# Kernel optimization log

Hardware: AMD Instinct MI355X
Metric: run time of the kernel (lower is better)

The kernel has to match this reference:

```python
import jax, jax.numpy as jnp
import numpy as np

B, F, N, L, K = 16, 256, 16384, 4096, 9  # batch, channels, input pixels, pooled pixels, kernel


def setup_inputs() -> dict:
    key = jax.random.key(0)
    k1, k2 = jax.random.split(key, 2)
    input_images = jax.random.normal(k1, (B, F, N), dtype=jnp.float32)
    # raw indices in [-1, N-1]; -1 marks a missing neighbor (zero padding)
    raw = jax.random.randint(k2, (L, K), 0, N + 1) - 1
    mask = (raw != -1).astype(jnp.float32)          # prepare_mask: mask out -1 entries
    indices = jnp.maximum(raw, 0)                   # prepare_mask: clamp -1 -> 0
    return {"input_images": input_images, "indices": indices, "mask": mask}


def reference(input_images, indices, mask):
    # gather neighbor features: (B, F, L, K)
    col = input_images[..., indices] * mask
    # max over kernel (neighbor) axis -> pooled image (B, F, L)
    return jnp.max(col, axis=-1)
```

## Files before the change

### kernel.cpp

```cpp
#include <hip/hip_runtime.h>

#define B_ 16
#define F_ 256
#define N_ 16384
#define L_ 4096
#define K_ 9

#define NTHR 256

typedef const __attribute__((address_space(1))) void* gas_ptr;
typedef __attribute__((address_space(3))) void* las_ptr;

__global__ __launch_bounds__(256) void prep_comb_kernel(
    const int* __restrict__ idx, const float* __restrict__ mask,
    unsigned short* __restrict__ comb) {
  int t = blockIdx.x * blockDim.x + threadIdx.x;
  if (t >= L_ * K_) return;
  int l = t / K_;
  int k = t - l * K_;
  comb[k * L_ + l] =
      (mask[t] != 0.0f) ? (unsigned short)idx[t] : (unsigned short)N_;
}

__global__ __launch_bounds__(NTHR) void pool_kernel(
    const float* __restrict__ img, const unsigned short* __restrict__ comb,
    float* __restrict__ out) {
  __shared__ __align__(16) float row[N_ + 4];
  const int bf = blockIdx.x;
  const int tid = threadIdx.x;
  const int lane = tid & 63;
  const int wv = tid >> 6;

  const float* src = img + (size_t)bf * N_;
#pragma unroll
  for (int i = 0; i < 16; ++i) {
    const int c = i * 4 + wv;
    const float* g = src + c * 256 + lane * 4;
    __builtin_amdgcn_global_load_lds((gas_ptr)g, (las_ptr)(row + c * 256),
                                     16, 0, 0);
  }
  if (tid == 0) row[N_] = 0.0f;
  __syncthreads();

  float* outp = out + (size_t)bf * L_;
#pragma unroll
  for (int it = 0; it < L_ / NTHR; ++it) {
    int l = it * NTHR + tid;
    float m = -INFINITY;
#pragma unroll
    for (int k = 0; k < K_; ++k) {
      int id = comb[k * L_ + l];
      m = fmaxf(m, row[id]);
    }
    outp[l] = m;
  }
}

__global__ __launch_bounds__(256) void pool_kernel_direct(
    const float* __restrict__ img, const int* __restrict__ idx,
    const float* __restrict__ mask, float* __restrict__ out) {
  __shared__ __align__(16) float row[N_ + 4];
  const int bf = blockIdx.x;
  const int tid = threadIdx.x;

  const float4* src4 = (const float4*)(img + (size_t)bf * N_);
  float4* row4 = (float4*)row;
#pragma unroll
  for (int i = 0; i < 16; ++i) {
    int j = i * 256 + tid;
    row4[j] = src4[j];
  }
  __syncthreads();

  float* outp = out + (size_t)bf * L_;
  for (int it = 0; it < L_ / 256; ++it) {
    int l = it * 256 + tid;
    float m = -INFINITY;
#pragma unroll
    for (int k = 0; k < K_; ++k) {
      int t = l * K_ + k;
      float v = (mask[t] != 0.0f) ? row[idx[t]] : 0.0f;
      m = fmaxf(m, v);
    }
    outp[l] = m;
  }
}

extern "C" void kernel_launch(void* const* d_in, const int* in_sizes, int n_in,
                              void* d_out, int out_size, void* d_ws, size_t ws_size,
                              hipStream_t stream) {
  const float* img = (const float*)d_in[0];
  const int* idx = (const int*)d_in[1];
  const float* mask = (const float*)d_in[2];
  float* out = (float*)d_out;

  const size_t comb_bytes = (size_t)L_ * K_ * sizeof(unsigned short);
  if (ws_size >= comb_bytes) {
    unsigned short* comb = (unsigned short*)d_ws;
    int total = L_ * K_;
    prep_comb_kernel<<<(total + 255) / 256, 256, 0, stream>>>(idx, mask, comb);
    pool_kernel<<<B_ * F_, NTHR, 0, stream>>>(img, comb, out);
  } else {
    pool_kernel_direct<<<B_ * F_, 256, 0, stream>>>(img, idx, mask, out);
  }
}
```

Before: 79.64 us.

## Make pooling kernel persistent with double-buffered LDS row prefetch

Replaces the one-block-per-(batch,channel) launch with 256 persistent 1024-thread blocks. Each block handles 16 rows, and the async global-to-LDS load of the next row overlaps with the gather/max over the current row in a second LDS buffer. The 9-way max is also rebalanced into a shallower tree after all gathers are issued. The aim is to hide row-load latency and cut per-block launch and ramp-up costs. In exchange, 128KB of LDS per block allows only one block per CU, and each row step needs a block-wide barrier.

```diff
diff --git a/kernel.cpp b/kernel.cpp
--- a/kernel.cpp
+++ b/kernel.cpp
@@ -6,7 +6,9 @@
 #define L_ 4096
 #define K_ 9
 
-#define NTHR 256
+#define NTHR 1024
+#define NBLK 256
+#define ROWS_PER_BLK (B_ * F_ / NBLK)
 
 typedef const __attribute__((address_space(1))) void* gas_ptr;
 typedef __attribute__((address_space(3))) void* las_ptr;
@@ -22,38 +24,57 @@
       (mask[t] != 0.0f) ? (unsigned short)idx[t] : (unsigned short)N_;
 }
 
-__global__ __launch_bounds__(NTHR) void pool_kernel(
+__global__ __launch_bounds__(NTHR) void pool_pipe_kernel(
     const float* __restrict__ img, const unsigned short* __restrict__ comb,
     float* __restrict__ out) {
-  __shared__ __align__(16) float row[N_ + 4];
-  const int bf = blockIdx.x;
+  __shared__ __align__(16) float buf[2][N_ + 16];
   const int tid = threadIdx.x;
+  const int bid = blockIdx.x;
   const int lane = tid & 63;
   const int wv = tid >> 6;
 
-  const float* src = img + (size_t)bf * N_;
-#pragma unroll
-  for (int i = 0; i < 16; ++i) {
-    const int c = i * 4 + wv;
-    const float* g = src + c * 256 + lane * 4;
-    __builtin_amdgcn_global_load_lds((gas_ptr)g, (las_ptr)(row + c * 256),
-                                     16, 0, 0);
+#define STAGE_ROW(row_, dstbuf_)                                         \
+  {                                                                      \
+    const float* src_ = img + (size_t)(row_)*N_;                         \
+    _Pragma("unroll") for (int i_ = 0; i_ < 4; ++i_) {                   \
+      const int c_ = i_ * 16 + wv;                                       \
+      __builtin_amdgcn_global_load_lds((gas_ptr)(src_ + c_ * 256 + lane * 4), \
+                                       (las_ptr)((dstbuf_) + c_ * 256),  \
+                                       16, 0, 0);                        \
+    }                                                                    \
   }
-  if (tid == 0) row[N_] = 0.0f;
+
+  STAGE_ROW(bid, &buf[0][0]);
+  if (tid < 2) buf[tid][N_] = 0.0f;
   __syncthreads();
 
-  float* outp = out + (size_t)bf * L_;
+#pragma unroll 1
+  for (int p = 0; p < ROWS_PER_BLK; ++p) {
+    if (p + 1 < ROWS_PER_BLK) {
+      const int nrow = (p + 1) * NBLK + bid;
+      STAGE_ROW(nrow, &buf[(p + 1) & 1][0]);
+    }
+
+    const float* row = &buf[p & 1][0];
+    float* outp = out + (size_t)((size_t)p * NBLK + bid) * L_;
 #pragma unroll
-  for (int it = 0; it < L_ / NTHR; ++it) {
-    int l = it * NTHR + tid;
-    float m = -INFINITY;
+    for (int it = 0; it < L_ / NTHR; ++it) {
+      int l = it * NTHR + tid;
+      float v[K_];
 #pragma unroll
-    for (int k = 0; k < K_; ++k) {
-      int id = comb[k * L_ + l];
-      m = fmaxf(m, row[id]);
+      for (int k = 0; k < K_; ++k) {
+        int id = comb[k * L_ + l];
+        v[k] = row[id];
+      }
+      float t0 = fmaxf(fmaxf(v[0], v[1]), v[2]);
+      float t1 = fmaxf(fmaxf(v[3], v[4]), v[5]);
+      float t2 = fmaxf(fmaxf(v[6], v[7]), v[8]);
+      outp[l] = fmaxf(fmaxf(t0, t1), t2);
     }
-    outp[l] = m;
+
+    __syncthreads();
   }
+#undef STAGE_ROW
 }
 
 __global__ __launch_bounds__(256) void pool_kernel_direct(
@@ -99,7 +120,7 @@
     unsigned short* comb = (unsigned short*)d_ws;
     int total = L_ * K_;
     prep_comb_kernel<<<(total + 255) / 256, 256, 0, stream>>>(idx, mask, comb);
-    pool_kernel<<<B_ * F_, NTHR, 0, stream>>>(img, comb, out);
+    pool_pipe_kernel<<<NBLK, NTHR, 0, stream>>>(img, comb, out);
   } else {
     pool_kernel_direct<<<B_ * F_, 256, 0, stream>>>(img, idx, mask, out);
   }
```

New measurement: 73.85 us. 1.08x faster.
